# Performance work log

Measured on AMD Instinct MI355X. Metric: run time of the kernel, lower is better.

Reference implementation:

```python
import jax, jax.numpy as jnp
import numpy as np

N_NODES = 50000
N_EDGES = 800000
NFEAT, NHID, NCLASS = 512, 128, 16


def _with_self_loops(edge_idx, n):
    loop = jnp.arange(n, dtype=edge_idx.dtype)
    src = jnp.concatenate([edge_idx[0], loop])  # [E+N]
    dst = jnp.concatenate([edge_idx[1], loop])
    return src, dst


def gcn_conv(x, src, dst, W, b, n):
    # GCNConv with add aggregation, self-loops, symmetric normalization.
    h = x @ W  # [N, out]
    ones = jnp.ones(src.shape[0], dtype=h.dtype)
    deg = jax.ops.segment_sum(ones, dst, num_segments=n)  # in-degree incl. self-loops
    dinv = jnp.where(deg > 0, jax.lax.rsqrt(deg), 0.0)
    norm = dinv[src] * dinv[dst]  # [E+N]
    msg = h[src] * norm[:, None]  # gather + scale
    out = jax.ops.segment_sum(msg, dst, num_segments=n)  # scatter-add
    return out + b


def setup_inputs() -> dict:
    key = jax.random.key(0)
    ks = jax.random.split(key, 8)
    x = jax.random.normal(ks[0], (N_NODES, NFEAT), dtype=jnp.float32)
    edge_idx = jax.random.randint(ks[1], (2, N_EDGES), 0, N_NODES, dtype=jnp.int64)
    s1 = 1.0 / np.sqrt(NFEAT)
    s2 = 1.0 / np.sqrt(NHID)
    W1 = jax.random.uniform(ks[2], (NFEAT, NHID), jnp.float32, -s1, s1)
    b1 = jnp.zeros((NHID,), jnp.float32)
    W2 = jax.random.uniform(ks[3], (NHID, NHID), jnp.float32, -s2, s2)
    b2 = jnp.zeros((NHID,), jnp.float32)
    Wc = jax.random.uniform(ks[4], (NHID, NCLASS), jnp.float32, -s2, s2)
    bc = jax.random.uniform(ks[5], (NCLASS,), jnp.float32, -s2, s2)
    return {"x": x, "edge_idx": edge_idx, "W1": W1, "b1": b1, "W2": W2, "b2": b2, "Wc": Wc, "bc": bc}


def reference(x, edge_idx, W1, b1, W2, b2, Wc, bc):
    n = x.shape[0]
    src, dst = _with_self_loops(edge_idx, n)
    h = gcn_conv(x, src, dst, W1, b1, n)
    h = jax.nn.relu(h)  # dropout is identity in eval mode
    h = gcn_conv(h, src, dst, W2, b2, n)
    h = jax.nn.relu(h)
    logits = h @ Wc + bc
    return jax.nn.log_softmax(logits, axis=1)
```

## Files before the change

### kernel.cpp

```cpp
#include <hip/hip_runtime.h>
#include <math.h>

#define NFEAT 512
#define NHID  128
#define NCLASS 16
#define SCAN_BS 512
#define AGG_BLOCKS 1024
#define NSTREAMS 16384

typedef __attribute__((ext_vector_type(8))) short short8;
typedef __attribute__((ext_vector_type(4))) float f32x4;

static __device__ __forceinline__ ushort f2b(float f) {
    union { float f; uint u; } v; v.f = f;
    uint r = v.u + 0x7FFFu + ((v.u >> 16) & 1u);
    return (ushort)(r >> 16);
}
static __device__ __forceinline__ float b2f_lo(uint bits) {
    union { uint u; float f; } v; v.u = bits << 16; return v.f;
}
static __device__ __forceinline__ float b2f_hi(uint bits) {
    union { uint u; float f; } v; v.u = bits & 0xffff0000u; return v.f;
}


__global__ void k_init_tcast(const float* __restrict__ W1, const float* __restrict__ W2,
                             ushort* __restrict__ W1T, ushort* __restrict__ W2T,
                             int* __restrict__ deg, int n) {
    int idx = blockIdx.x * 256 + threadIdx.x;
    if (idx < n) deg[idx] = 1;
    if (idx < NFEAT * 128) {
        int k = idx >> 7, c = idx & 127;
        W1T[(size_t)c * NFEAT + k] = f2b(W1[idx]);
    } else {
        int j = idx - NFEAT * 128;
        if (j < NHID * 128) {
            int k = j >> 7, c = j & 127;
            W2T[(size_t)c * NHID + k] = f2b(W2[j]);
        }
    }
}

__global__ void k_count(const int* __restrict__ dst, int e, int* __restrict__ deg) {
    int i = blockIdx.x * blockDim.x + threadIdx.x;
    if (i < e) atomicAdd(&deg[dst[i]], 1);
}

__global__ void k_scan1(const int* __restrict__ deg, float* __restrict__ dinv,
                        int* __restrict__ cursor, int* __restrict__ offs,
                        int* __restrict__ bsum, int n) {
    __shared__ int s[SCAN_BS];
    int t = threadIdx.x;
    int i = blockIdx.x * SCAN_BS + t;
    int d = (i < n) ? deg[i] : 0;
    if (i < n) { dinv[i] = rsqrtf((float)d); cursor[i] = 0; }
    s[t] = d;
    for (int off = 1; off < SCAN_BS; off <<= 1) {
        __syncthreads();
        int x = (t >= off) ? s[t - off] : 0;
        __syncthreads();
        s[t] += x;
    }
    __syncthreads();
    if (i < n) offs[i] = s[t] - d;
    if (t == SCAN_BS - 1) bsum[blockIdx.x] = s[t];
}

__global__ void k_scan2(int* __restrict__ bsum, int* __restrict__ offs, int nb, int n) {
    int lane = threadIdx.x;
    int carry = 0;
    for (int base = 0; base < nb; base += 64) {
        int i = base + lane;
        int v = (i < nb) ? bsum[i] : 0;
        int orig = v;
        for (int off = 1; off < 64; off <<= 1) {
            int t = __shfl_up(v, off);
            if (lane >= off) v += t;
        }
        if (i < nb) bsum[i] = carry + v - orig;
        carry += __shfl(v, 63);
    }
    if (lane == 0) offs[n] = carry;
}

__global__ void k_scan3(int* __restrict__ offs, const int* __restrict__ bsum, int n) {
    int i = blockIdx.x * SCAN_BS + threadIdx.x;
    if (i < n) offs[i] += bsum[blockIdx.x];
}

__global__ void k_fill_edges(const int* __restrict__ src, const int* __restrict__ dst, int e,
                             const int* __restrict__ eoffs, int* __restrict__ cursor,
                             uint* __restrict__ colp32, int n, int S) {
    int i = blockIdx.x * blockDim.x + threadIdx.x;
    if (i < e) {
        int d = dst[i];
        int p = atomicAdd(&cursor[d], 1);
        colp32[eoffs[d] + p] = (uint)src[i];
    }
    if (i < n) {
        colp32[eoffs[i + 1] - 1] = (uint)i | ((uint)(i + 1) << 16);
    }
    if (i == 0) {
#pragma unroll
        for (int k = 0; k < 8; k++) colp32[S + k] = 0;
    }
}

__global__ void k_rankstart(const uint* __restrict__ colp32, int* __restrict__ rankgs, int S) {
    int r = blockIdx.x * blockDim.x + threadIdx.x;
    if (r >= NSTREAMS) return;
    int len = (S + NSTREAMS - 1) / NSTREAMS;
    int g = r * len;
    int ge = g + len; if (ge > S) ge = S;
    if (g >= S) { rankgs[r] = -1; return; }
    if (g > 0) {
        while (g < ge && !(colp32[g - 1] >> 16)) g++;
        if (g >= ge) { rankgs[r] = -1; return; }
    }
    rankgs[r] = g;
}


template<int A_F32>
__global__ __launch_bounds__(256) void k_gemm(const void* __restrict__ Aptr,
                                              const ushort* __restrict__ WT,
                                              const float* __restrict__ rowscale,
                                              ushort* __restrict__ Hs, int M, int K) {
    __shared__ ushort As[64][40];
    __shared__ ushort Bs[128][40];

    const int tid = threadIdx.x;
    const int wc = tid >> 6, lane = tid & 63;
    const int lr = lane & 15, lk = (lane >> 4) * 8;
    const int rowbase = blockIdx.x * 64;

    f32x4 acc[4][2];
#pragma unroll
    for (int i = 0; i < 4; i++)
#pragma unroll
        for (int j = 0; j < 2; j++) acc[i][j] = (f32x4)0.f;

    const int sr = tid >> 2;
    const int sh = (tid & 3) * 8;

    for (int k0 = 0; k0 < K; k0 += 32) {
        {
            int gr = rowbase + sr;
            ushort tmp[8];
            if (A_F32) {
                const float* A = (const float*)Aptr;
                if (gr < M) {
                    const float* p = A + (size_t)gr * K + k0 + sh;
#pragma unroll
                    for (int q = 0; q < 2; q++) {
                        float4 v = *(const float4*)(p + q * 4);
                        tmp[q * 4 + 0] = f2b(v.x); tmp[q * 4 + 1] = f2b(v.y);
                        tmp[q * 4 + 2] = f2b(v.z); tmp[q * 4 + 3] = f2b(v.w);
                    }
                } else {
#pragma unroll
                    for (int q = 0; q < 8; q++) tmp[q] = 0;
                }
            } else {
                const ushort* A = (const ushort*)Aptr;
                if (gr < M) {
                    *(short8*)&tmp[0] = *(const short8*)(A + (size_t)gr * K + k0 + sh);
                } else {
#pragma unroll
                    for (int q = 0; q < 8; q++) tmp[q] = 0;
                }
            }
            *(short8*)&As[sr][sh] = *(short8*)&tmp[0];
        }
        {
#pragma unroll
            for (int t = 0; t < 2; t++) {
                int c = tid + t * 256;
                int row = c >> 2, q = c & 3;
                short8 v = *(const short8*)(WT + (size_t)row * K + k0 + q * 8);
                *(short8*)&Bs[row][q * 8] = v;
            }
        }
        __syncthreads();

        short8 af[4], bfv[2];
#pragma unroll
        for (int i = 0; i < 4; i++) af[i] = *(const short8*)&As[i * 16 + lr][lk];
#pragma unroll
        for (int j = 0; j < 2; j++) bfv[j] = *(const short8*)&Bs[wc * 32 + j * 16 + lr][lk];
#pragma unroll
        for (int i = 0; i < 4; i++)
#pragma unroll
            for (int j = 0; j < 2; j++)
                acc[i][j] = __builtin_amdgcn_mfma_f32_16x16x32_bf16(af[i], bfv[j], acc[i][j], 0, 0, 0);
        __syncthreads();
    }

#pragma unroll
    for (int i = 0; i < 4; i++) {
#pragma unroll
        for (int r = 0; r < 4; r++) {
            int row = rowbase + i * 16 + (lane >> 4) * 4 + r;
            if (row < M) {
                float sc = rowscale[row];
#pragma unroll
                for (int j = 0; j < 2; j++) {
                    int f = j * 16 + lr;
                    Hs[((size_t)wc * M + row) * 32 + f] = f2b(acc[i][j][r] * sc);
                }
            }
        }
    }
}


__global__ __launch_bounds__(256) void k_aggs(const ushort* __restrict__ hs,
                                              const uint* __restrict__ colp32,
                                              const int* __restrict__ rankgs,
                                              const float* __restrict__ dinv,
                                              const float* __restrict__ bias,
                                              ushort* __restrict__ outp, int n, int S) {
    const int b = blockIdx.x;
    const int s = b & 3;
    const int wid = threadIdx.x >> 6, lane = threadIdx.x & 63;
    const int st16 = lane >> 2, q = lane & 3;
    const int stream = (((b >> 2) << 2) + wid) * 16 + st16;
    const int len = (S + NSTREAMS - 1) / NSTREAMS;
    int gs = rankgs[stream];
    int ge = (stream + 1) * len; if (ge > S) ge = S;
    bool alive = (gs >= 0);
    int g = alive ? gs : 0;

    const ushort* hsl = hs + (size_t)s * n * 32;
    const float4 bv0 = *(const float4*)(bias + s * 32 + q * 8);
    const float4 bv1 = *(const float4*)(bias + s * 32 + q * 8 + 4);

    const uint* cp = colp32 + g;
    uint cw0 = cp[0], cw1 = cp[1], cw2 = cp[2];
    uint4 pk0 = *(const uint4*)(hsl + (size_t)(cw0 & 0xffffu) * 32 + q * 8);
    uint4 pk1 = *(const uint4*)(hsl + (size_t)(cw1 & 0xffffu) * 32 + q * 8);
    float fdv0 = (cw0 >> 16) ? dinv[(cw0 >> 16) - 1] : 0.f;
    float fdv1 = (cw1 >> 16) ? dinv[(cw1 >> 16) - 1] : 0.f;
    float a0 = 0.f, a1 = 0.f, a2 = 0.f, a3 = 0.f;
    float a4 = 0.f, a5 = 0.f, a6 = 0.f, a7 = 0.f;

    while (__any(alive)) {
        if (alive) {
            uint cw3 = cp[3];
            uint4 pk2 = *(const uint4*)(hsl + (size_t)(cw2 & 0xffffu) * 32 + q * 8);
            float fdv2 = (cw2 >> 16) ? dinv[(cw2 >> 16) - 1] : 0.f;

            a0 += b2f_lo(pk0.x); a1 += b2f_hi(pk0.x);
            a2 += b2f_lo(pk0.y); a3 += b2f_hi(pk0.y);
            a4 += b2f_lo(pk0.z); a5 += b2f_hi(pk0.z);
            a6 += b2f_lo(pk0.w); a7 += b2f_hi(pk0.w);

            if (cw0 >> 16) {
                int v = (int)(cw0 >> 16) - 1;
                float r0 = fmaxf(fmaf(a0, fdv0, bv0.x), 0.f);
                float r1 = fmaxf(fmaf(a1, fdv0, bv0.y), 0.f);
                float r2 = fmaxf(fmaf(a2, fdv0, bv0.z), 0.f);
                float r3 = fmaxf(fmaf(a3, fdv0, bv0.w), 0.f);
                float r4 = fmaxf(fmaf(a4, fdv0, bv1.x), 0.f);
                float r5 = fmaxf(fmaf(a5, fdv0, bv1.y), 0.f);
                float r6 = fmaxf(fmaf(a6, fdv0, bv1.z), 0.f);
                float r7 = fmaxf(fmaf(a7, fdv0, bv1.w), 0.f);
                uint4 u;
                u.x = (uint)f2b(r0) | ((uint)f2b(r1) << 16);
                u.y = (uint)f2b(r2) | ((uint)f2b(r3) << 16);
                u.z = (uint)f2b(r4) | ((uint)f2b(r5) << 16);
                u.w = (uint)f2b(r6) | ((uint)f2b(r7) << 16);
                *(uint4*)(outp + (size_t)v * 128 + s * 32 + q * 8) = u;
                a0 = a1 = a2 = a3 = a4 = a5 = a6 = a7 = 0.f;
                if (g + 1 >= ge) alive = false;
            }
            g++; cp++;
            cw0 = cw1; cw1 = cw2; cw2 = cw3;
            pk0 = pk1; pk1 = pk2;
            fdv0 = fdv1; fdv1 = fdv2;
        }
    }
}


__global__ __launch_bounds__(256) void k_classify(const ushort* __restrict__ h,
                                                  const float* __restrict__ Wc,
                                                  const float* __restrict__ bc,
                                                  float* __restrict__ out, int n) {
    __shared__ float Ws[128 * 16];
    int tid = threadIdx.x;
#pragma unroll
    for (int t = 0; t < 8; t++) Ws[tid + 256 * t] = Wc[tid + 256 * t];
    __syncthreads();

    int wid = tid >> 6, lane = tid & 63;
    int v = blockIdx.x * 4 + wid;
    if (v >= n) return;

    int j = lane & 15, c = lane >> 4;
    const ushort* hv = h + (size_t)v * 128 + c * 32;
    float acc = 0.f;
#pragma unroll
    for (int t = 0; t < 16; t++) {
        uint pk = *(const uint*)(hv + t * 2);
        acc = fmaf(b2f_lo(pk), Ws[(c * 32 + t * 2 + 0) * 16 + j], acc);
        acc = fmaf(b2f_hi(pk), Ws[(c * 32 + t * 2 + 1) * 16 + j], acc);
    }
    acc += __shfl_xor(acc, 16);
    acc += __shfl_xor(acc, 32);
    acc += bc[j];

    float m = acc;
#pragma unroll
    for (int o = 8; o >= 1; o >>= 1) m = fmaxf(m, __shfl_xor(m, o));
    float sum = expf(acc - m);
#pragma unroll
    for (int o = 8; o >= 1; o >>= 1) sum += __shfl_xor(sum, o);
    if (lane < 16) out[(size_t)v * 16 + j] = acc - m - logf(sum);
}


extern "C" void kernel_launch(void* const* d_in, const int* in_sizes, int n_in,
                              void* d_out, int out_size, void* d_ws, size_t ws_size,
                              hipStream_t stream) {
    const float* x  = (const float*)d_in[0];
    const int* eidx = (const int*)d_in[1];
    const float* W1 = (const float*)d_in[2];
    const float* b1 = (const float*)d_in[3];
    const float* W2 = (const float*)d_in[4];
    const float* b2 = (const float*)d_in[5];
    const float* Wc = (const float*)d_in[6];
    const float* bc = (const float*)d_in[7];
    float* out = (float*)d_out;

    const int N = in_sizes[0] / NFEAT;
    const int E = in_sizes[1] / 2;
    const int S = E + N;
    const int* src = eidx;
    const int* dst = eidx + E;

    char* p = (char*)d_ws;
    auto alloc = [&](size_t bytes) { char* r = p; p += (bytes + 255) & ~(size_t)255; return r; };
    int*    deg    = (int*)   alloc((size_t)N * 4);
    float*  dinv   = (float*) alloc((size_t)N * 4);
    int*    eoffs  = (int*)   alloc((size_t)(N + 1) * 4);
    int*    cursor = (int*)   alloc((size_t)N * 4);
    uint*   colp32 = (uint*)  alloc(((size_t)S + 16) * 4);
    int*    rankgs = (int*)   alloc((size_t)NSTREAMS * 4);
    int*    bsum   = (int*)   alloc((size_t)256 * 4);
    ushort* W1T    = (ushort*)alloc((size_t)128 * NFEAT * 2);
    ushort* W2T    = (ushort*)alloc((size_t)128 * NHID * 2);
    ushort* hs     = (ushort*)alloc((size_t)N * NHID * 2);
    ushort* g1     = (ushort*)alloc((size_t)N * NHID * 2);
    ushort* g2     = (ushort*)alloc((size_t)N * NHID * 2);

    const int nb = (N + SCAN_BS - 1) / SCAN_BS;

    k_init_tcast<<<((NFEAT + NHID) * 128 + 255) / 256, 256, 0, stream>>>(W1, W2, W1T, W2T, deg, N);
    k_count<<<(E + 255) / 256, 256, 0, stream>>>(dst, E, deg);
    k_scan1<<<nb, SCAN_BS, 0, stream>>>(deg, dinv, cursor, eoffs, bsum, N);
    k_scan2<<<1, 64, 0, stream>>>(bsum, eoffs, nb, N);
    k_scan3<<<nb, SCAN_BS, 0, stream>>>(eoffs, bsum, N);
    k_fill_edges<<<(E + 255) / 256, 256, 0, stream>>>(src, dst, E, eoffs, cursor, colp32, N, S);
    k_rankstart<<<(NSTREAMS + 255) / 256, 256, 0, stream>>>(colp32, rankgs, S);

    const int gblocks = (N + 63) / 64;
    k_gemm<1><<<gblocks, 256, 0, stream>>>(x, W1T, dinv, hs, N, NFEAT);
    k_aggs<<<AGG_BLOCKS, 256, 0, stream>>>(hs, colp32, rankgs, dinv, b1, g1, N, S);
    k_gemm<0><<<gblocks, 256, 0, stream>>>(g1, W2T, dinv, hs, N, NHID);
    k_aggs<<<AGG_BLOCKS, 256, 0, stream>>>(hs, colp32, rankgs, dinv, b2, g2, N, S);
    k_classify<<<(N + 3) / 4, 256, 0, stream>>>(g2, Wc, bc, out, N);
}
```

Measured before the change: 260.6 us.

## Fuse CSR build kernels, use atomic tickets, binary-search stream starts, deepen prefetch

Each edge now keeps the ticket returned by its degree-count atomic. The fill pass places edges using that ticket instead of a second atomic on a cursor array, so the cursor array goes away. The separate block-sum scan kernel is folded into the offset-add kernel, and the stream-start search is folded into the fill kernel as a binary search over row offsets, which removes two launches and a serial pass over colp32. The aggregation loop prefetches one more neighbor row, adding latency hiding at the cost of more registers. Every block of k_scan3 now redundantly scans the block sums, and a per-edge ticket buffer is added.

```diff
diff --git a/kernel.cpp b/kernel.cpp
--- a/kernel.cpp
+++ b/kernel.cpp
@@ -41,19 +41,19 @@
     }
 }
 
-__global__ void k_count(const int* __restrict__ dst, int e, int* __restrict__ deg) {
+__global__ void k_count(const int* __restrict__ dst, int e, int* __restrict__ deg,
+                        int* __restrict__ ticket) {
     int i = blockIdx.x * blockDim.x + threadIdx.x;
-    if (i < e) atomicAdd(&deg[dst[i]], 1);
+    if (i < e) ticket[i] = atomicAdd(&deg[dst[i]], 1);
 }
 
 __global__ void k_scan1(const int* __restrict__ deg, float* __restrict__ dinv,
-                        int* __restrict__ cursor, int* __restrict__ offs,
-                        int* __restrict__ bsum, int n) {
+                        int* __restrict__ offs, int* __restrict__ bsum, int n) {
     __shared__ int s[SCAN_BS];
     int t = threadIdx.x;
     int i = blockIdx.x * SCAN_BS + t;
     int d = (i < n) ? deg[i] : 0;
-    if (i < n) { dinv[i] = rsqrtf((float)d); cursor[i] = 0; }
+    if (i < n) dinv[i] = rsqrtf((float)d);
     s[t] = d;
     for (int off = 1; off < SCAN_BS; off <<= 1) {
         __syncthreads();
@@ -66,58 +66,55 @@
     if (t == SCAN_BS - 1) bsum[blockIdx.x] = s[t];
 }
 
-__global__ void k_scan2(int* __restrict__ bsum, int* __restrict__ offs, int nb, int n) {
-    int lane = threadIdx.x;
-    int carry = 0;
-    for (int base = 0; base < nb; base += 64) {
-        int i = base + lane;
-        int v = (i < nb) ? bsum[i] : 0;
-        int orig = v;
-        for (int off = 1; off < 64; off <<= 1) {
-            int t = __shfl_up(v, off);
-            if (lane >= off) v += t;
-        }
-        if (i < nb) bsum[i] = carry + v - orig;
-        carry += __shfl(v, 63);
-    }
-    if (lane == 0) offs[n] = carry;
-}
-
-__global__ void k_scan3(int* __restrict__ offs, const int* __restrict__ bsum, int n) {
-    int i = blockIdx.x * SCAN_BS + threadIdx.x;
-    if (i < n) offs[i] += bsum[blockIdx.x];
+__global__ void k_scan3(int* __restrict__ offs, const int* __restrict__ bsum, int nb, int n) {
+    __shared__ int pref[128];
+    int t = threadIdx.x;
+    if (t < 64) {
+        int carry = 0;
+        for (int base = 0; base < nb; base += 64) {
+            int j = base + t;
+            int v = (j < nb) ? bsum[j] : 0;
+            for (int off = 1; off < 64; off <<= 1) {
+                int x = __shfl_up(v, off);
+                if (t >= off) v += x;
+            }
+            if (j < nb) pref[j] = carry + v;
+            carry += __shfl(v, 63);
+        }
+    }
+    __syncthreads();
+    int i = blockIdx.x * SCAN_BS + t;
+    int add = blockIdx.x ? pref[blockIdx.x - 1] : 0;
+    if (i < n) offs[i] += add;
+    if (blockIdx.x == 0 && t == 0) offs[n] = pref[nb - 1];
 }
 
 __global__ void k_fill_edges(const int* __restrict__ src, const int* __restrict__ dst, int e,
-                             const int* __restrict__ eoffs, int* __restrict__ cursor,
-                             uint* __restrict__ colp32, int n, int S) {
+                             const int* __restrict__ eoffs, const int* __restrict__ ticket,
+                             uint* __restrict__ colp32, int* __restrict__ rankgs,
+                             int n, int S) {
     int i = blockIdx.x * blockDim.x + threadIdx.x;
     if (i < e) {
-        int d = dst[i];
-        int p = atomicAdd(&cursor[d], 1);
-        colp32[eoffs[d] + p] = (uint)src[i];
+        colp32[eoffs[dst[i]] + ticket[i] - 1] = (uint)src[i];
     }
     if (i < n) {
         colp32[eoffs[i + 1] - 1] = (uint)i | ((uint)(i + 1) << 16);
     }
+    if (i < NSTREAMS) {
+        int len = (S + NSTREAMS - 1) / NSTREAMS;
+        int target = i * len;
+        int lo = 0, hi = n;
+        while (lo < hi) {
+            int mid = (lo + hi) >> 1;
+            if (eoffs[mid] < target) lo = mid + 1; else hi = mid;
+        }
+        rankgs[i] = eoffs[lo];
+        if (i == 0) rankgs[NSTREAMS] = S;
+    }
     if (i == 0) {
 #pragma unroll
         for (int k = 0; k < 8; k++) colp32[S + k] = 0;
     }
-}
-
-__global__ void k_rankstart(const uint* __restrict__ colp32, int* __restrict__ rankgs, int S) {
-    int r = blockIdx.x * blockDim.x + threadIdx.x;
-    if (r >= NSTREAMS) return;
-    int len = (S + NSTREAMS - 1) / NSTREAMS;
-    int g = r * len;
-    int ge = g + len; if (ge > S) ge = S;
-    if (g >= S) { rankgs[r] = -1; return; }
-    if (g > 0) {
-        while (g < ge && !(colp32[g - 1] >> 16)) g++;
-        if (g >= ge) { rankgs[r] = -1; return; }
-    }
-    rankgs[r] = g;
 }
 
 
@@ -219,36 +216,37 @@
                                               const int* __restrict__ rankgs,
                                               const float* __restrict__ dinv,
                                               const float* __restrict__ bias,
-                                              ushort* __restrict__ outp, int n, int S) {
+                                              ushort* __restrict__ outp, int n) {
     const int b = blockIdx.x;
     const int s = b & 3;
     const int wid = threadIdx.x >> 6, lane = threadIdx.x & 63;
     const int st16 = lane >> 2, q = lane & 3;
     const int stream = (((b >> 2) << 2) + wid) * 16 + st16;
-    const int len = (S + NSTREAMS - 1) / NSTREAMS;
     int gs = rankgs[stream];
-    int ge = (stream + 1) * len; if (ge > S) ge = S;
-    bool alive = (gs >= 0);
-    int g = alive ? gs : 0;
+    int se = rankgs[stream + 1];
+    bool alive = gs < se;
+    int g = gs;
 
     const ushort* hsl = hs + (size_t)s * n * 32;
     const float4 bv0 = *(const float4*)(bias + s * 32 + q * 8);
     const float4 bv1 = *(const float4*)(bias + s * 32 + q * 8 + 4);
 
     const uint* cp = colp32 + g;
-    uint cw0 = cp[0], cw1 = cp[1], cw2 = cp[2];
+    uint cw0 = cp[0], cw1 = cp[1], cw2 = cp[2], cw3 = cp[3];
     uint4 pk0 = *(const uint4*)(hsl + (size_t)(cw0 & 0xffffu) * 32 + q * 8);
     uint4 pk1 = *(const uint4*)(hsl + (size_t)(cw1 & 0xffffu) * 32 + q * 8);
+    uint4 pk2 = *(const uint4*)(hsl + (size_t)(cw2 & 0xffffu) * 32 + q * 8);
     float fdv0 = (cw0 >> 16) ? dinv[(cw0 >> 16) - 1] : 0.f;
     float fdv1 = (cw1 >> 16) ? dinv[(cw1 >> 16) - 1] : 0.f;
+    float fdv2 = (cw2 >> 16) ? dinv[(cw2 >> 16) - 1] : 0.f;
     float a0 = 0.f, a1 = 0.f, a2 = 0.f, a3 = 0.f;
     float a4 = 0.f, a5 = 0.f, a6 = 0.f, a7 = 0.f;
 
     while (__any(alive)) {
         if (alive) {
-            uint cw3 = cp[3];
-            uint4 pk2 = *(const uint4*)(hsl + (size_t)(cw2 & 0xffffu) * 32 + q * 8);
-            float fdv2 = (cw2 >> 16) ? dinv[(cw2 >> 16) - 1] : 0.f;
+            uint cw4 = cp[4];
+            uint4 pk3 = *(const uint4*)(hsl + (size_t)(cw3 & 0xffffu) * 32 + q * 8);
+            float fdv3 = (cw3 >> 16) ? dinv[(cw3 >> 16) - 1] : 0.f;
 
             a0 += b2f_lo(pk0.x); a1 += b2f_hi(pk0.x);
             a2 += b2f_lo(pk0.y); a3 += b2f_hi(pk0.y);
@@ -272,12 +270,12 @@
                 u.w = (uint)f2b(r6) | ((uint)f2b(r7) << 16);
                 *(uint4*)(outp + (size_t)v * 128 + s * 32 + q * 8) = u;
                 a0 = a1 = a2 = a3 = a4 = a5 = a6 = a7 = 0.f;
-                if (g + 1 >= ge) alive = false;
+                if (g + 1 >= se) alive = false;
             }
             g++; cp++;
-            cw0 = cw1; cw1 = cw2; cw2 = cw3;
-            pk0 = pk1; pk1 = pk2;
-            fdv0 = fdv1; fdv1 = fdv2;
+            cw0 = cw1; cw1 = cw2; cw2 = cw3; cw3 = cw4;
+            pk0 = pk1; pk1 = pk2; pk2 = pk3;
+            fdv0 = fdv1; fdv1 = fdv2; fdv2 = fdv3;
         }
     }
 }
@@ -344,9 +342,9 @@
     int*    deg    = (int*)   alloc((size_t)N * 4);
     float*  dinv   = (float*) alloc((size_t)N * 4);
     int*    eoffs  = (int*)   alloc((size_t)(N + 1) * 4);
-    int*    cursor = (int*)   alloc((size_t)N * 4);
+    int*    ticket = (int*)   alloc((size_t)E * 4);
     uint*   colp32 = (uint*)  alloc(((size_t)S + 16) * 4);
-    int*    rankgs = (int*)   alloc((size_t)NSTREAMS * 4);
+    int*    rankgs = (int*)   alloc((size_t)(NSTREAMS + 1) * 4);
     int*    bsum   = (int*)   alloc((size_t)256 * 4);
     ushort* W1T    = (ushort*)alloc((size_t)128 * NFEAT * 2);
     ushort* W2T    = (ushort*)alloc((size_t)128 * NHID * 2);
@@ -357,17 +355,16 @@
     const int nb = (N + SCAN_BS - 1) / SCAN_BS;
 
     k_init_tcast<<<((NFEAT + NHID) * 128 + 255) / 256, 256, 0, stream>>>(W1, W2, W1T, W2T, deg, N);
-    k_count<<<(E + 255) / 256, 256, 0, stream>>>(dst, E, deg);
-    k_scan1<<<nb, SCAN_BS, 0, stream>>>(deg, dinv, cursor, eoffs, bsum, N);
-    k_scan2<<<1, 64, 0, stream>>>(bsum, eoffs, nb, N);
-    k_scan3<<<nb, SCAN_BS, 0, stream>>>(eoffs, bsum, N);
-    k_fill_edges<<<(E + 255) / 256, 256, 0, stream>>>(src, dst, E, eoffs, cursor, colp32, N, S);
-    k_rankstart<<<(NSTREAMS + 255) / 256, 256, 0, stream>>>(colp32, rankgs, S);
+    k_count<<<(E + 255) / 256, 256, 0, stream>>>(dst, E, deg, ticket);
+    k_scan1<<<nb, SCAN_BS, 0, stream>>>(deg, dinv, eoffs, bsum, N);
+    k_scan3<<<nb, SCAN_BS, 0, stream>>>(eoffs, bsum, nb, N);
+    k_fill_edges<<<(E + 255) / 256, 256, 0, stream>>>(src, dst, E, eoffs, ticket, colp32,
+                                                      rankgs, N, S);
 
     const int gblocks = (N + 63) / 64;
     k_gemm<1><<<gblocks, 256, 0, stream>>>(x, W1T, dinv, hs, N, NFEAT);
-    k_aggs<<<AGG_BLOCKS, 256, 0, stream>>>(hs, colp32, rankgs, dinv, b1, g1, N, S);
+    k_aggs<<<AGG_BLOCKS, 256, 0, stream>>>(hs, colp32, rankgs, dinv, b1, g1, N);
     k_gemm<0><<<gblocks, 256, 0, stream>>>(g1, W2T, dinv, hs, N, NHID);
-    k_aggs<<<AGG_BLOCKS, 256, 0, stream>>>(hs, colp32, rankgs, dinv, b2, g2, N, S);
+    k_aggs<<<AGG_BLOCKS, 256, 0, stream>>>(hs, colp32, rankgs, dinv, b2, g2, N);
     k_classify<<<(N + 3) / 4, 256, 0, stream>>>(g2, Wc, bc, out, N);
 }
```

Measured after the change: 227.7 us. 1.14x faster.
